# Kernel optimization log

Hardware: AMD Instinct MI355X
Metric: run time of the kernel (lower is better)

Reference implementation:

```python
import jax, jax.numpy as jnp
import numpy as np

NEG_SLOPE = 0.2  # PyG GATConv default leaky_relu slope


def gat_conv(x, edge_index, W, a_src, a_dst, b):
    """PyG GATConv (heads=1, concat=True, add_self_loops=True, dropout=0)."""
    N = x.shape[0]
    loops = jnp.arange(N, dtype=edge_index.dtype)
    src = jnp.concatenate([edge_index[0], loops])  # [Ef]
    dst = jnp.concatenate([edge_index[1], loops])  # [Ef]
    h = x @ W  # [N, Dout]
    alpha_src = h @ a_src  # [N]
    alpha_dst = h @ a_dst  # [N]
    logits = jax.nn.leaky_relu(alpha_src[src] + alpha_dst[dst], NEG_SLOPE)  # [Ef]
    # segment softmax over edges grouped by destination node
    m = jax.ops.segment_max(logits, dst, num_segments=N)
    e = jnp.exp(logits - m[dst])
    denom = jax.ops.segment_sum(e, dst, num_segments=N)  # >0: every node has a self-loop
    alpha = e / denom[dst]  # [Ef]
    out = jax.ops.segment_sum(alpha[:, None] * h[src], dst, num_segments=N)
    return out + b


def global_mean_pool(x, batch, num_graphs):
    s = jax.ops.segment_sum(x, batch, num_segments=num_graphs)
    cnt = jax.ops.segment_sum(jnp.ones((x.shape[0],), x.dtype), batch, num_segments=num_graphs)
    return s / jnp.maximum(cnt, 1.0)[:, None]


NUM_GRAPHS = 64


def setup_inputs() -> dict:
    key = jax.random.key(0)
    ks = jax.random.split(key, 12)
    N, E, D = 50000, 600000, 128
    x = jax.random.normal(ks[0], (N, D), dtype=jnp.float32)
    edge_index = jax.random.randint(ks[1], (2, E), 0, N, dtype=jnp.int32)
    edge_weight = jax.random.uniform(ks[2], (E,), dtype=jnp.float32)
    batch = jnp.sort(jax.random.randint(ks[3], (N,), 0, NUM_GRAPHS, dtype=jnp.int32))
    sc = 1.0 / np.sqrt(D)
    W0 = jax.random.normal(ks[4], (D, D), dtype=jnp.float32) * sc
    a_src0 = jax.random.normal(ks[5], (D,), dtype=jnp.float32) * sc
    a_dst0 = jax.random.normal(ks[6], (D,), dtype=jnp.float32) * sc
    b0 = jnp.zeros((D,), dtype=jnp.float32)
    W1 = jax.random.normal(ks[7], (D, D), dtype=jnp.float32) * sc
    a_src1 = jax.random.normal(ks[8], (D,), dtype=jnp.float32) * sc
    a_dst1 = jax.random.normal(ks[9], (D,), dtype=jnp.float32) * sc
    b1 = jnp.zeros((D,), dtype=jnp.float32)
    return {"x": x, "edge_index": edge_index, "edge_weight": edge_weight, "batch": batch,
            "W0": W0, "a_src0": a_src0, "a_dst0": a_dst0, "b0": b0,
            "W1": W1, "a_src1": a_src1, "a_dst1": a_dst1, "b1": b1}


def reference(x, edge_index, edge_weight, batch, W0, a_src0, a_dst0, b0, W1, a_src1, a_dst1, b1):
    # layer 0 (relu_layers_index=[0] -> ReLU after layer 0)
    out = gat_conv(x, edge_index, W0, a_src0, a_dst0, b0)
    out = jax.nn.relu(out)
    emb0 = global_mean_pool(out, batch, NUM_GRAPHS)
    # layer 1 (no relu, no dropout)
    out = gat_conv(out, edge_index, W1, a_src1, a_dst1, b1)
    emb1 = global_mean_pool(out, batch, NUM_GRAPHS)
    return (emb0, emb1)
```

## Files before the change

### kernel.cpp

```cpp
#include <hip/hip_runtime.h>

typedef unsigned int u32;
typedef unsigned short u16;

typedef short bf16x8 __attribute__((ext_vector_type(8)));
typedef float f32x4 __attribute__((ext_vector_type(4)));
typedef float f32x2 __attribute__((ext_vector_type(2)));

__device__ __forceinline__ float bl(u32 u){ return __uint_as_float(u << 16); }
__device__ __forceinline__ float bh(u32 u){ return __uint_as_float(u & 0xffff0000u); }
__device__ __forceinline__ float b16f(u16 r){ return __uint_as_float(((u32)r) << 16); }
__device__ __forceinline__ u16 f2b(float f){
  u32 u = __float_as_uint(f);
  u32 r = (u + 0x7fffu + ((u >> 16) & 1u)) >> 16;
  return (u16)r;
}
__device__ __forceinline__ u32 pk2(float a, float b){
  return (u32)f2b(a) | ((u32)f2b(b) << 16);
}
__device__ __forceinline__ void fma8(float* acc, float e2, uint2 h){
  f32x2 p0 = __builtin_amdgcn_cvt_pk_f32_fp8((int)h.x, 0);
  f32x2 p1 = __builtin_amdgcn_cvt_pk_f32_fp8((int)h.x, 1);
  f32x2 p2 = __builtin_amdgcn_cvt_pk_f32_fp8((int)h.y, 0);
  f32x2 p3 = __builtin_amdgcn_cvt_pk_f32_fp8((int)h.y, 1);
  acc[0]=fmaf(e2,p0.x,acc[0]); acc[1]=fmaf(e2,p0.y,acc[1]);
  acc[2]=fmaf(e2,p1.x,acc[2]); acc[3]=fmaf(e2,p1.y,acc[3]);
  acc[4]=fmaf(e2,p2.x,acc[4]); acc[5]=fmaf(e2,p2.y,acc[5]);
  acc[6]=fmaf(e2,p3.x,acc[6]); acc[7]=fmaf(e2,p3.y,acc[7]);
}

#define NEG_SLOPE 0.2f
#define CAP 64


__device__ __forceinline__ int block_detect(const u32* __restrict__ x){
  __shared__ int cnt_;
  if (threadIdx.x == 0) cnt_ = 0;
  __syncthreads();
  u32 w = x[threadIdx.x];
  int e = (int)((w >> 7) & 0xFFu);
  if (e >= 110 && e <= 135) atomicAdd(&cnt_, 1);
  __syncthreads();
  return (cnt_ >= 128) ? 1 : 0;
}

template<bool XEXT, bool KPERM>
__device__ __forceinline__ void gemm_body(int gb, int isbf,
    const void* __restrict__ Xv, const void* __restrict__ Wv,
    const void* __restrict__ av, const void* __restrict__ dv,
    u32* __restrict__ Hb, float* __restrict__ As, float* __restrict__ Ad, int N)
{
  __shared__ u16 Wt[128*136];
  const int tid = threadIdx.x;

  if (isbf){
    const u32* Wp = (const u32*)Wv;
    #pragma unroll
    for (int i = 0; i < 16; i++){
      int idx = tid + i*256;
      u32 p = Wp[idx];
      int k = idx >> 6, n2 = idx & 63;
      int pos = KPERM ? ((k & 15)*8 + (k >> 4)) : k;
      Wt[(2*n2)*136 + pos]   = (u16)(p & 0xffffu);
      Wt[(2*n2+1)*136 + pos] = (u16)(p >> 16);
    }
  } else {
    const float* Wf = (const float*)Wv;
    #pragma unroll
    for (int i = 0; i < 64; i++){
      int idx = tid + i*256;
      int k = idx >> 7, n = idx & 127;
      int pos = KPERM ? ((k & 15)*8 + (k >> 4)) : k;
      Wt[n*136 + pos] = f2b(Wf[idx]);
    }
  }
  __syncthreads();

  const int wv = tid >> 6, L = tid & 63;
  const int row0 = (gb*4 + wv) * 16;
  if (row0 >= N) return;
  const int nl = L & 15, quad = L >> 4;

  bf16x8 af[4];
  if (!XEXT || isbf){
    const uint4* Xr = (const uint4*)(((const u32*)Xv) + (long)row0*64);
    #pragma unroll
    for (int kb = 0; kb < 4; kb++)
      af[kb] = *(const bf16x8*)&Xr[nl*16 + kb*4 + quad];
  } else {
    const float* Xf = ((const float*)Xv) + (long)(row0 + nl)*128;
    #pragma unroll
    for (int kb = 0; kb < 4; kb++){
      const float4* p = (const float4*)(Xf + kb*32 + quad*8);
      float4 f0 = p[0], f1 = p[1];
      uint4 tmp = make_uint4(pk2(f0.x,f0.y), pk2(f0.z,f0.w), pk2(f1.x,f1.y), pk2(f1.z,f1.w));
      af[kb] = *(const bf16x8*)&tmp;
    }
  }

  f32x4 acc[8];
  #pragma unroll
  for (int nt = 0; nt < 8; nt++) acc[nt] = (f32x4){0.f,0.f,0.f,0.f};
  #pragma unroll
  for (int nt = 0; nt < 8; nt++){
    #pragma unroll
    for (int kb = 0; kb < 4; kb++){
      bf16x8 bf = *(const bf16x8*)&Wt[(nt*16 + nl)*136 + kb*32 + quad*8];
      acc[nt] = __builtin_amdgcn_mfma_f32_16x16x32_bf16(af[kb], bf, acc[nt], 0, 0, 0);
    }
  }

  float ps[4] = {0.f,0.f,0.f,0.f}, pd[4] = {0.f,0.f,0.f,0.f};
  #pragma unroll
  for (int nt = 0; nt < 8; nt++){
    int col = nt*16 + nl;
    float a_ = isbf ? b16f(((const u16*)av)[col]) : ((const float*)av)[col];
    float d_ = isbf ? b16f(((const u16*)dv)[col]) : ((const float*)dv)[col];
    #pragma unroll
    for (int r = 0; r < 4; r++){
      ps[r] = fmaf(acc[nt][r], a_, ps[r]);
      pd[r] = fmaf(acc[nt][r], d_, pd[r]);
    }
  }
  #pragma unroll
  for (int off = 1; off < 16; off <<= 1){
    #pragma unroll
    for (int r = 0; r < 4; r++){
      ps[r] += __shfl_xor(ps[r], off);
      pd[r] += __shfl_xor(pd[r], off);
    }
  }
  if (nl == 0){
    #pragma unroll
    for (int r = 0; r < 4; r++){
      As[row0 + quad*4 + r] = ps[r];
      Ad[row0 + quad*4 + r] = pd[r];
    }
  }

  #pragma unroll
  for (int r = 0; r < 4; r++){
    long row = row0 + quad*4 + r;
    int w0 = 0, w1 = 0;
    w0 = __builtin_amdgcn_cvt_pk_fp8_f32(acc[0][r], acc[1][r], w0, 0);
    w0 = __builtin_amdgcn_cvt_pk_fp8_f32(acc[2][r], acc[3][r], w0, 1);
    w1 = __builtin_amdgcn_cvt_pk_fp8_f32(acc[4][r], acc[5][r], w1, 0);
    w1 = __builtin_amdgcn_cvt_pk_fp8_f32(acc[6][r], acc[7][r], w1, 1);
    uint2 v = make_uint2((u32)w0, (u32)w1);
    *(uint2*)(Hb + row*32 + nl*2) = v;
  }
}

__device__ __forceinline__ void pool_body(const u32* __restrict__ Ob,
    const int* __restrict__ batch, float* __restrict__ psum, int N)
{
  const int tid = threadIdx.x;
  const int wv = tid >> 6, lane = tid & 63;
  const int start = blockIdx.x * 128;
  const int end = min(start + 128, N);
  float2 acc = make_float2(0.f, 0.f);
  int cur = -1;
  for (int node = start + wv; node < end; node += 4){
    int gid = batch[node];
    if (gid != cur){
      if (cur >= 0){
        atomicAdd(&psum[cur*128 + lane*2],     acc.x);
        atomicAdd(&psum[cur*128 + lane*2 + 1], acc.y);
      }
      cur = gid; acc = make_float2(0.f, 0.f);
    }
    u32 p = Ob[(long)node*64 + lane];
    acc.x += bl(p); acc.y += bh(p);
  }
  if (cur >= 0){
    atomicAdd(&psum[cur*128 + lane*2],     acc.x);
    atomicAdd(&psum[cur*128 + lane*2 + 1], acc.y);
  }
}

__global__ __launch_bounds__(256) void scatgemm0_k(
    const int* __restrict__ ei, int* __restrict__ deg, int* __restrict__ csrc, int E, int eB,
    const u32* __restrict__ x, int* __restrict__ flag,
    const void* __restrict__ W0, const void* __restrict__ as0, const void* __restrict__ ad0,
    u32* __restrict__ Hb, float* __restrict__ As, float* __restrict__ Ad, int N)
{
  if ((int)blockIdx.x < eB){
    int t = blockIdx.x*256 + threadIdx.x;
    if (t < E){
      int d = ei[E + t];
      int pos = atomicAdd(deg + d, 1);
      if (pos < CAP) csrc[d*CAP + pos] = ei[t];
    }
    return;
  }
  const int gb = blockIdx.x - eB;
  int isbf = block_detect(x);
  if (gb == 0 && threadIdx.x == 0) *flag = isbf;
  gemm_body<true, false>(gb, isbf, x, W0, as0, ad0, Hb, As, Ad, N);
}

__global__ __launch_bounds__(256) void poolgemm1_k(
    const u32* __restrict__ Ob, const int* __restrict__ batch, float* __restrict__ ps0, int pB,
    const void* __restrict__ W1, const void* __restrict__ as1, const void* __restrict__ ad1,
    const int* __restrict__ flag,
    u32* __restrict__ Hb, float* __restrict__ As, float* __restrict__ Ad, int N)
{
  if ((int)blockIdx.x < pB){
    pool_body(Ob, batch, ps0, N);
    return;
  }
  const int gb = blockIdx.x - pB;
  gemm_body<false, true>(gb, *flag, Ob, W1, as1, ad1, Hb, As, Ad, N);
}

template<bool RELU>
__global__ __launch_bounds__(256) void gath_k(const int* __restrict__ deg,
    const int* __restrict__ csrc, const float* __restrict__ As, const float* __restrict__ Ad,
    const u32* __restrict__ Hb, const void* __restrict__ bv, const int* __restrict__ flag,
    u32* __restrict__ Ob, int N)
{
  long t = (long)blockIdx.x*256 + threadIdx.x;
  int node = (int)(t >> 4), q = (int)(t & 15);
  if (node >= N) return;
  const int base = threadIdx.x & 48;
  const float ad = Ad[node];
  float l = As[node] + ad;
  l = l > 0.f ? l : NEG_SLOPE * l;
  float e = __expf(l);
  float acc[8];
  {
    uint2 hv = ((const uint2*)(Hb + (long)node*32))[q];
    f32x2 p0 = __builtin_amdgcn_cvt_pk_f32_fp8((int)hv.x, 0);
    f32x2 p1 = __builtin_amdgcn_cvt_pk_f32_fp8((int)hv.x, 1);
    f32x2 p2 = __builtin_amdgcn_cvt_pk_f32_fp8((int)hv.y, 0);
    f32x2 p3 = __builtin_amdgcn_cvt_pk_f32_fp8((int)hv.y, 1);
    acc[0]=e*p0.x; acc[1]=e*p0.y; acc[2]=e*p1.x; acc[3]=e*p1.y;
    acc[4]=e*p2.x; acc[5]=e*p2.y; acc[6]=e*p3.x; acc[7]=e*p3.y;
  }
  float den = e;
  int dg = deg[node]; if (dg > CAP) dg = CAP;
  const int* row = csrc + (long)node*CAP;
  for (int jb = 0; jb < dg; jb += 16){
    int m = dg - jb; if (m > 16) m = 16;
    int sj = node; float evq = 0.f;
    if (q < m){
      sj = row[jb + q];
      float l2 = As[sj] + ad;
      l2 = l2 > 0.f ? l2 : NEG_SLOPE * l2;
      evq = __expf(l2);
    }
    for (int i = 0; i < m; i += 4){
      float e0 = __shfl(evq, base + i);
      float e1 = __shfl(evq, base + i + 1);
      float e2 = __shfl(evq, base + i + 2);
      float e3 = __shfl(evq, base + i + 3);
      int   s0 = __shfl(sj,  base + i);
      int   s1 = __shfl(sj,  base + i + 1);
      int   s2 = __shfl(sj,  base + i + 2);
      int   s3 = __shfl(sj,  base + i + 3);
      uint2 h0 = ((const uint2*)(Hb + (long)s0*32))[q];
      uint2 h1 = ((const uint2*)(Hb + (long)s1*32))[q];
      uint2 h2 = ((const uint2*)(Hb + (long)s2*32))[q];
      uint2 h3 = ((const uint2*)(Hb + (long)s3*32))[q];
      den += (e0 + e1) + (e2 + e3);
      fma8(acc, e0, h0);
      fma8(acc, e1, h1);
      fma8(acc, e2, h2);
      fma8(acc, e3, h3);
    }
  }
  float inv = 1.f / den;
  float b[8];
  if (*flag){
    const u16* bp = (const u16*)bv;
    #pragma unroll
    for (int i = 0; i < 8; i++) b[i] = b16f(bp[i*16 + q]);
  } else {
    const float* bp = (const float*)bv;
    #pragma unroll
    for (int i = 0; i < 8; i++) b[i] = bp[i*16 + q];
  }
  float o[8];
  #pragma unroll
  for (int i = 0; i < 8; i++){
    o[i] = fmaf(acc[i], inv, b[i]);
    if (RELU) o[i] = fmaxf(o[i], 0.f);
  }
  uint4 w = make_uint4(pk2(o[0],o[1]), pk2(o[2],o[3]), pk2(o[4],o[5]), pk2(o[6],o[7]));
  *(uint4*)&Ob[(long)node*64 + q*4] = w;
}

__global__ __launch_bounds__(256) void pool2_k(const u32* __restrict__ Ob,
    const int* __restrict__ batch, float* __restrict__ psum, int N)
{
  pool_body(Ob, batch, psum, N);
}

__global__ __launch_bounds__(256) void fin_k(const float* __restrict__ ps0,
    const float* __restrict__ ps1, const int* __restrict__ batch, int N,
    const int* __restrict__ flag, void* __restrict__ out)
{
  int t = blockIdx.x*256 + threadIdx.x;
  if (t >= 8192) return;
  int g = t >> 7, pos = t & 127;
  int c = ((pos & 7) << 4) + (pos >> 3);
  int lo = 0, hi = N;
  while (lo < hi){ int mid = (lo + hi) >> 1; if (batch[mid] < g) lo = mid + 1; else hi = mid; }
  int a = lo;
  lo = 0; hi = N;
  while (lo < hi){ int mid = (lo + hi) >> 1; if (batch[mid] < g + 1) lo = mid + 1; else hi = mid; }
  int cc = lo - a;
  float cf = (float)(cc < 1 ? 1 : cc);
  float v0 = ps0[t] / cf, v1 = ps1[t] / cf;
  if (*flag){
    u16* o = (u16*)out;
    o[g*128 + c] = f2b(v0); o[8192 + g*128 + c] = f2b(v1);
  } else {
    float* o = (float*)out;
    o[g*128 + c] = v0; o[8192 + g*128 + c] = v1;
  }
}

extern "C" void kernel_launch(void* const* d_in, const int* in_sizes, int n_in,
                              void* d_out, int out_size, void* d_ws, size_t ws_size,
                              hipStream_t stream)
{
  const void* x    = d_in[0];
  const int* ei    = (const int*)d_in[1];
  const int* batch = (const int*)d_in[3];
  const void* W0  = d_in[4];
  const void* as0 = d_in[5];
  const void* ad0 = d_in[6];
  const void* b0  = d_in[7];
  const void* W1  = d_in[8];
  const void* as1 = d_in[9];
  const void* ad1 = d_in[10];
  const void* b1  = d_in[11];

  const int N  = in_sizes[0] / 128;
  const int E  = in_sizes[1] / 2;

  char* ws = (char*)d_ws;
  size_t off = 0;
  auto al = [&](size_t bytes){ size_t o = off; off += (bytes + 255) & ~(size_t)255; return o; };
  u32*   Hb    = (u32*)(ws + al((size_t)N*32*4));
  u32*   Ob    = (u32*)(ws + al((size_t)N*64*4));
  float* As    = (float*)(ws + al((size_t)N*4));
  float* Ad    = (float*)(ws + al((size_t)N*4));
  int*   csrc  = (int*)(ws + al((size_t)N*CAP*4));
  char*  z0    = ws + al((size_t)N*4 + 2*64*128*4);
  int*   deg   = (int*)z0;
  float* ps0   = (float*)(z0 + (size_t)N*4);
  float* ps1   = ps0 + 8192;
  int*   flag  = (int*)(ws + al(256));
  if (off > ws_size) return;

  hipMemsetAsync(deg, 0, (size_t)N*4 + 2*64*128*4, stream);

  const int gB   = (N/16 + 3) / 4;
  const int eB   = (E + 255) / 256;
  const int nvB16= (N*16 + 255) / 256;
  const int pB   = (N + 127) / 128;

  scatgemm0_k<<<eB + gB, 256, 0, stream>>>(ei, deg, csrc, E, eB,
      (const u32*)x, flag, W0, as0, ad0, Hb, As, Ad, N);
  gath_k<true><<<nvB16, 256, 0, stream>>>(deg, csrc, As, Ad, Hb, b0, flag, Ob, N);

  poolgemm1_k<<<pB + gB, 256, 0, stream>>>(Ob, batch, ps0, pB,
      W1, as1, ad1, flag, Hb, As, Ad, N);
  gath_k<false><<<nvB16, 256, 0, stream>>>(deg, csrc, As, Ad, Hb, b1, flag, Ob, N);
  pool2_k<<<pB, 256, 0, stream>>>(Ob, batch, ps1, N);

  fin_k<<<32, 256, 0, stream>>>(ps0, ps1, batch, N, flag, d_out);
}
```

Measured before the change: 208.8 us.

## Build CSR via two-pass bucketed partition instead of capped atomic scatter

Replaces the per-edge global atomic scatter into a fixed 64-slot-per-node adjacency with a two-kernel bucketed partition. Edges are first grouped into 256-node buckets through shared-memory histograms, then turned into a compact per-bucket CSR with a rowptr array. This is meant to cut global atomic contention and scattered writes, and it removes the degree cap, which was a correctness hazard. In exchange it adds a kernel launch, splits the GEMM out of the fused scatter kernel, and assumes no bucket exceeds 4096 edges.

```diff
diff --git a/kernel.cpp b/kernel.cpp
--- a/kernel.cpp
+++ b/kernel.cpp
@@ -2,6 +2,7 @@
 
 typedef unsigned int u32;
 typedef unsigned short u16;
+typedef unsigned long long u64;
 
 typedef short bf16x8 __attribute__((ext_vector_type(8)));
 typedef float f32x4 __attribute__((ext_vector_type(4)));
@@ -30,7 +31,7 @@
 }
 
 #define NEG_SLOPE 0.2f
-#define CAP 64
+#define BSTRIDE 4096
 
 
 __device__ __forceinline__ int block_detect(const u32* __restrict__ x){
@@ -42,6 +43,100 @@
   if (e >= 110 && e <= 135) atomicAdd(&cnt_, 1);
   __syncthreads();
   return (cnt_ >= 128) ? 1 : 0;
+}
+
+__global__ __launch_bounds__(256) void part_k(const int* __restrict__ ei, int E, int nbuck,
+    int* __restrict__ gcnt, u64* __restrict__ breg)
+{
+  __shared__ u32 hist[256];
+  __shared__ u32 lscan[257];
+  __shared__ u32 gbase[256];
+  __shared__ u32 cur[256];
+  __shared__ u64 stage[2048];
+  const int tid = threadIdx.x;
+  hist[tid] = 0; cur[tid] = 0;
+  __syncthreads();
+  const int e0 = blockIdx.x * 2048;
+  int src[8], dst[8];
+  #pragma unroll
+  for (int j = 0; j < 8; j++){
+    int t = e0 + tid + j*256;
+    if (t < E){
+      src[j] = ei[t]; dst[j] = ei[E + t];
+      atomicAdd(&hist[dst[j] >> 8], 1u);
+    } else dst[j] = -1;
+  }
+  __syncthreads();
+  const u32 v = hist[tid];
+  lscan[tid] = v;
+  __syncthreads();
+  for (int off = 1; off < 256; off <<= 1){
+    u32 add = (tid >= off) ? lscan[tid - off] : 0;
+    __syncthreads();
+    lscan[tid] += add;
+    __syncthreads();
+  }
+  if (tid == 255) lscan[256] = lscan[255];
+  u32 excl = lscan[tid] - v;
+  __syncthreads();
+  const u32 total = lscan[256];
+  lscan[tid] = excl;
+  if (tid < nbuck && v > 0) gbase[tid] = (u32)atomicAdd(&gcnt[tid], (int)v);
+  __syncthreads();
+  #pragma unroll
+  for (int j = 0; j < 8; j++){
+    if (dst[j] >= 0){
+      int b = dst[j] >> 8;
+      u32 p = lscan[b] + atomicAdd(&cur[b], 1u);
+      stage[p] = ((u64)(u32)dst[j] << 32) | (u32)src[j];
+    }
+  }
+  __syncthreads();
+  for (u32 i = tid; i < total; i += 256){
+    u64 e = stage[i];
+    int b = (int)(e >> 40);
+    u32 r = i - lscan[b];
+    breg[(long)b * BSTRIDE + gbase[b] + r] = e;
+  }
+}
+
+__global__ __launch_bounds__(256) void csr_k(const int* __restrict__ gcnt,
+    const u64* __restrict__ breg,
+    int* __restrict__ deg, int* __restrict__ rowptr, int* __restrict__ csrc, int N)
+{
+  __shared__ u32 dl[256];
+  __shared__ u32 rp[256];
+  __shared__ u32 cu[256];
+  const int b = blockIdx.x, tid = threadIdx.x;
+  const int n0 = b << 8;
+  const int cntb = gcnt[b];
+  dl[tid] = 0; cu[tid] = 0;
+  __syncthreads();
+  const u64* reg = breg + (long)b * BSTRIDE;
+  for (int i = tid; i < cntb; i += 256)
+    atomicAdd(&dl[(int)(reg[i] >> 32) - n0], 1u);
+  __syncthreads();
+  const u32 v = dl[tid];
+  rp[tid] = v;
+  __syncthreads();
+  for (int off = 1; off < 256; off <<= 1){
+    u32 add = (tid >= off) ? rp[tid - off] : 0;
+    __syncthreads();
+    rp[tid] += add;
+    __syncthreads();
+  }
+  u32 excl = rp[tid] - v;
+  __syncthreads();
+  rp[tid] = excl;
+  __syncthreads();
+  int node = n0 + tid;
+  if (node < N){ deg[node] = (int)v; rowptr[node] = b*BSTRIDE + (int)excl; }
+  for (int i = tid; i < cntb; i += 256){
+    u64 e = reg[i];
+    int d = (int)(e >> 32) - n0;
+    u32 pos = rp[d] + atomicAdd(&cu[d], 1u);
+    csrc[(long)b*BSTRIDE + pos] = (int)(e & 0xffffffffULL);
+  }
 }
 
 template<bool XEXT, bool KPERM>
@@ -178,25 +273,14 @@
   }
 }
 
-__global__ __launch_bounds__(256) void scatgemm0_k(
-    const int* __restrict__ ei, int* __restrict__ deg, int* __restrict__ csrc, int E, int eB,
+__global__ __launch_bounds__(256) void gemmdet0_k(
     const u32* __restrict__ x, int* __restrict__ flag,
     const void* __restrict__ W0, const void* __restrict__ as0, const void* __restrict__ ad0,
     u32* __restrict__ Hb, float* __restrict__ As, float* __restrict__ Ad, int N)
 {
-  if ((int)blockIdx.x < eB){
-    int t = blockIdx.x*256 + threadIdx.x;
-    if (t < E){
-      int d = ei[E + t];
-      int pos = atomicAdd(deg + d, 1);
-      if (pos < CAP) csrc[d*CAP + pos] = ei[t];
-    }
-    return;
-  }
-  const int gb = blockIdx.x - eB;
   int isbf = block_detect(x);
-  if (gb == 0 && threadIdx.x == 0) *flag = isbf;
-  gemm_body<true, false>(gb, isbf, x, W0, as0, ad0, Hb, As, Ad, N);
+  if (blockIdx.x == 0 && threadIdx.x == 0) *flag = isbf;
+  gemm_body<true, false>(blockIdx.x, isbf, x, W0, as0, ad0, Hb, As, Ad, N);
 }
 
 __global__ __launch_bounds__(256) void poolgemm1_k(
@@ -209,13 +293,13 @@
     pool_body(Ob, batch, ps0, N);
     return;
   }
-  const int gb = blockIdx.x - pB;
-  gemm_body<false, true>(gb, *flag, Ob, W1, as1, ad1, Hb, As, Ad, N);
+  gemm_body<false, true>(blockIdx.x - pB, *flag, Ob, W1, as1, ad1, Hb, As, Ad, N);
 }
 
 template<bool RELU>
 __global__ __launch_bounds__(256) void gath_k(const int* __restrict__ deg,
-    const int* __restrict__ csrc, const float* __restrict__ As, const float* __restrict__ Ad,
+    const int* __restrict__ rowptr, const int* __restrict__ csrc,
+    const float* __restrict__ As, const float* __restrict__ Ad,
     const u32* __restrict__ Hb, const void* __restrict__ bv, const int* __restrict__ flag,
     u32* __restrict__ Ob, int N)
 {
@@ -238,8 +322,8 @@
     acc[4]=e*p2.x; acc[5]=e*p2.y; acc[6]=e*p3.x; acc[7]=e*p3.y;
   }
   float den = e;
-  int dg = deg[node]; if (dg > CAP) dg = CAP;
-  const int* row = csrc + (long)node*CAP;
+  const int dg = deg[node];
+  const int* row = csrc + rowptr[node];
   for (int jb = 0; jb < dg; jb += 16){
     int m = dg - jb; if (m > 16) m = 16;
     int sj = node; float evq = 0.f;
@@ -339,6 +423,7 @@
 
   const int N  = in_sizes[0] / 128;
   const int E  = in_sizes[1] / 2;
+  const int nbuck = (N + 255) >> 8;
 
   char* ws = (char*)d_ws;
   size_t off = 0;
@@ -347,28 +432,33 @@
   u32*   Ob    = (u32*)(ws + al((size_t)N*64*4));
   float* As    = (float*)(ws + al((size_t)N*4));
   float* Ad    = (float*)(ws + al((size_t)N*4));
-  int*   csrc  = (int*)(ws + al((size_t)N*CAP*4));
-  char*  z0    = ws + al((size_t)N*4 + 2*64*128*4);
-  int*   deg   = (int*)z0;
-  float* ps0   = (float*)(z0 + (size_t)N*4);
+  u64*   breg  = (u64*)(ws + al((size_t)nbuck*BSTRIDE*8));
+  int*   csrc  = (int*)(ws + al((size_t)nbuck*BSTRIDE*4));
+  int*   deg   = (int*)(ws + al((size_t)N*4));
+  int*   rowptr= (int*)(ws + al((size_t)N*4));
+  char*  z0    = ws + al(2*64*128*4 + 256*4);
+  float* ps0   = (float*)z0;
   float* ps1   = ps0 + 8192;
+  int*   gcnt  = (int*)(ps1 + 8192);
   int*   flag  = (int*)(ws + al(256));
   if (off > ws_size) return;
 
-  hipMemsetAsync(deg, 0, (size_t)N*4 + 2*64*128*4, stream);
+  hipMemsetAsync(z0, 0, 2*64*128*4 + 256*4, stream);
 
   const int gB   = (N/16 + 3) / 4;
-  const int eB   = (E + 255) / 256;
+  const int aB   = (E + 2047) / 2048;
   const int nvB16= (N*16 + 255) / 256;
   const int pB   = (N + 127) / 128;
 
-  scatgemm0_k<<<eB + gB, 256, 0, stream>>>(ei, deg, csrc, E, eB,
-      (const u32*)x, flag, W0, as0, ad0, Hb, As, Ad, N);
-  gath_k<true><<<nvB16, 256, 0, stream>>>(deg, csrc, As, Ad, Hb, b0, flag, Ob, N);
+  gemmdet0_k<<<gB, 256, 0, stream>>>((const u32*)x, flag, W0, as0, ad0, Hb, As, Ad, N);
+  part_k<<<aB, 256, 0, stream>>>(ei, E, nbuck, gcnt, breg);
+  csr_k<<<nbuck, 256, 0, stream>>>(gcnt, breg, deg, rowptr, csrc, N);
+
+  gath_k<true><<<nvB16, 256, 0, stream>>>(deg, rowptr, csrc, As, Ad, Hb, b0, flag, Ob, N);
 
   poolgemm1_k<<<pB + gB, 256, 0, stream>>>(Ob, batch, ps0, pB,
       W1, as1, ad1, flag, Hb, As, Ad, N);
-  gath_k<false><<<nvB16, 256, 0, stream>>>(deg, csrc, As, Ad, Hb, b1, flag, Ob, N);
+  gath_k<false><<<nvB16, 256, 0, stream>>>(deg, rowptr, csrc, As, Ad, Hb, b1, flag, Ob, N);
   pool2_k<<<pB, 256, 0, stream>>>(Ob, batch, ps1, N);
 
   fin_k<<<32, 256, 0, stream>>>(ps0, ps1, batch, N, flag, d_out);
```

New measurement: 196.8 us (median of 2 runs). -5.7%, faster.
